# Kernel tuning notes

Measured on AMD Instinct MI355X. Metric: run time of the kernel, lower is better.

Reference implementation:

```python
import jax, jax.numpy as jnp
import numpy as np

B, S, H, A = 64, 4096, 256, 128


def entmax15(z):
    # exact entmax-1.5 along the last axis (Peters & Martins 2019)
    z = z / 2.0
    z = z - jnp.max(z, axis=-1, keepdims=True)
    zs = -jnp.sort(-z, axis=-1)                      # descending sort
    n = zs.shape[-1]
    k = jnp.arange(1, n + 1, dtype=z.dtype)
    mean = jnp.cumsum(zs, axis=-1) / k
    mean_sq = jnp.cumsum(zs * zs, axis=-1) / k
    ss = k * (mean_sq - mean * mean)
    delta = jnp.clip((1.0 - ss) / k, 0.0)
    tau = mean - jnp.sqrt(delta)
    k_star = jnp.sum(tau <= zs, axis=-1)             # support size per row
    tau_star = jnp.take_along_axis(tau, (k_star - 1)[..., None], axis=-1)
    return jnp.square(jnp.clip(z - tau_star, 0.0))


def setup_inputs() -> dict:
    key = jax.random.key(0)
    k0, k1, k2, k3, k4 = jax.random.split(key, 5)
    lim1 = 1.0 / np.sqrt(H)
    lim2 = 1.0 / np.sqrt(A)
    return {
        "lstm_output": jax.random.normal(k0, (B, S, H), dtype=jnp.float32),
        "W1": jax.random.uniform(k1, (H, A), jnp.float32, -lim1, lim1),
        "b1": jax.random.uniform(k2, (A,), jnp.float32, -lim1, lim1),
        "W2": jax.random.uniform(k3, (A, 1), jnp.float32, -lim2, lim2),
        "b2": jax.random.uniform(k4, (1,), jnp.float32, -lim2, lim2),
    }


def reference(lstm_output, W1, b1, W2, b2):
    # score MLP: Linear -> Tanh -> Linear -> squeeze(-1)  => [B, S]
    h = jnp.tanh(jnp.einsum("bsh,ha->bsa", lstm_output, W1) + b1)
    scores = (jnp.einsum("bsa,ao->bso", h, W2) + b2)[..., 0]
    weights = entmax15(scores)                       # entmax over seq axis (dim=1)
    context = jnp.einsum("bsh,bs->bh", lstm_output, weights)
    return (context, weights)
```

## Files before the change

kernel.cpp:

```cpp
#include <hip/hip_runtime.h>
#include <hip/hip_bf16.h>

#define BB 64
#define SS 4096
#define HH 256
#define AA 128
#define MT 128
#define BK 64
#define XST 72

typedef __fp16 fp16v2 __attribute__((ext_vector_type(2)));
typedef _Float16 half4v __attribute__((ext_vector_type(4)));
typedef _Float16 half8v __attribute__((ext_vector_type(8)));
typedef float floatx16 __attribute__((ext_vector_type(16)));

__device__ __forceinline__ float fast_tanh(float x) {
    float xc = fminf(fmaxf(x, -9.0f), 9.0f);
    float e = __expf(2.0f * xc);
    return 1.0f - __fdividef(2.0f, e + 1.0f);
}

__global__ void convert_w1(const float* __restrict__ W1, _Float16* __restrict__ Wt) {
    int n = blockIdx.x;
    int k = threadIdx.x;
    Wt[n * HH + k] = (_Float16)W1[k * AA + n];
}

__global__ __launch_bounds__(256) void score_mfma(
    const float* __restrict__ X,
    const _Float16* __restrict__ Wt,
    const float* __restrict__ b1,
    const float* __restrict__ W2,
    const float* __restrict__ b2,
    float* __restrict__ scores)
{
    __shared__ float smem_f[9216];
    _Float16* Xs = (_Float16*)smem_f;
    _Float16* Ws = (_Float16*)smem_f + MT * XST;
    float* part = smem_f;

    const int tid   = threadIdx.x;
    const int m0    = blockIdx.x * MT;
    const int wid   = tid >> 6;
    const int lane  = tid & 63;
    const int lrow  = lane & 31;
    const int lhalf = lane >> 5;
    const int wr    = (wid & 1) * 64;
    const int wc    = (wid >> 1) * 64;

    floatx16 acc[2][2];
    #pragma unroll
    for (int i = 0; i < 2; ++i)
        #pragma unroll
        for (int j = 0; j < 2; ++j)
            #pragma unroll
            for (int r = 0; r < 16; ++r) acc[i][j][r] = 0.0f;

    float4 xv[8];
    uint4  wvv[4];

#define LOAD_CHUNK(K0)                                                         \
    do {                                                                       \
        _Pragma("unroll")                                                      \
        for (int p = 0; p < 8; ++p) {                                          \
            int idx = tid + p * 256;                                           \
            int row = idx >> 4, c4 = idx & 15;                                 \
            xv[p] = *(const float4*)(X + (size_t)(m0 + row) * HH + (K0) + c4 * 4); \
        }                                                                      \
        _Pragma("unroll")                                                      \
        for (int p = 0; p < 4; ++p) {                                          \
            int idx = tid + p * 256;                                           \
            int n = idx >> 3, u = idx & 7;                                     \
            wvv[p] = *(const uint4*)(Wt + (size_t)n * HH + (K0) + u * 8);      \
        }                                                                      \
    } while (0)

#define STORE_CHUNK()                                                          \
    do {                                                                       \
        _Pragma("unroll")                                                      \
        for (int p = 0; p < 8; ++p) {                                          \
            int idx = tid + p * 256;                                           \
            int row = idx >> 4, c4 = idx & 15;                                 \
            union { fp16v2 h2[2]; half4v h4; } u;                              \
            u.h2[0] = __builtin_amdgcn_cvt_pkrtz(xv[p].x, xv[p].y);            \
            u.h2[1] = __builtin_amdgcn_cvt_pkrtz(xv[p].z, xv[p].w);            \
            *(half4v*)(Xs + row * XST + c4 * 4) = u.h4;                        \
        }                                                                      \
        _Pragma("unroll")                                                      \
        for (int p = 0; p < 4; ++p) {                                          \
            int idx = tid + p * 256;                                           \
            int n = idx >> 3, u2 = idx & 7;                                    \
            *(uint4*)(Ws + n * XST + u2 * 8) = wvv[p];                         \
        }                                                                      \
    } while (0)

    LOAD_CHUNK(0);
    STORE_CHUNK();
    __syncthreads();

    #pragma unroll
    for (int c = 0; c < HH / BK; ++c) {
        if (c + 1 < HH / BK) LOAD_CHUNK((c + 1) * BK);
        #pragma unroll
        for (int kk = 0; kk < BK; kk += 16) {
            half8v a0 = *(half8v*)(Xs + (wr + lrow) * XST + kk + lhalf * 8);
            half8v a1 = *(half8v*)(Xs + (wr + 32 + lrow) * XST + kk + lhalf * 8);
            half8v b0 = *(half8v*)(Ws + (wc + lrow) * XST + kk + lhalf * 8);
            half8v bq = *(half8v*)(Ws + (wc + 32 + lrow) * XST + kk + lhalf * 8);
            acc[0][0] = __builtin_amdgcn_mfma_f32_32x32x16_f16(a0, b0, acc[0][0], 0, 0, 0);
            acc[0][1] = __builtin_amdgcn_mfma_f32_32x32x16_f16(a0, bq, acc[0][1], 0, 0, 0);
            acc[1][0] = __builtin_amdgcn_mfma_f32_32x32x16_f16(a1, b0, acc[1][0], 0, 0, 0);
            acc[1][1] = __builtin_amdgcn_mfma_f32_32x32x16_f16(a1, bq, acc[1][1], 0, 0, 0);
        }
        __syncthreads();
        if (c + 1 < HH / BK) {
            STORE_CHUNK();
            __syncthreads();
        }
    }
#undef LOAD_CHUNK
#undef STORE_CHUNK

    const int cA = wc + lrow;
    const int cB = wc + 32 + lrow;
    const float b1A = b1[cA], b1B = b1[cB];
    const float w2A = W2[cA], w2B = W2[cB];
    #pragma unroll
    for (int i = 0; i < 2; ++i) {
        #pragma unroll
        for (int r = 0; r < 16; ++r) {
            float hA = fast_tanh(acc[i][0][r] + b1A) * w2A;
            float hB = fast_tanh(acc[i][1][r] + b1B) * w2B;
            int row = wr + i * 32 + (r & 3) + 8 * (r >> 2) + 4 * lhalf;
            part[row * 65 + (wid >> 1) * 32 + lrow] = hA + hB;
        }
    }
    __syncthreads();
    if (tid < MT) {
        float s = b2[0];
        #pragma unroll
        for (int c = 0; c < 64; ++c) s += part[tid * 65 + c];
        scores[m0 + tid] = s;
    }
}

__global__ __launch_bounds__(256) void entmax_kernel(
    float* __restrict__ buf, float* __restrict__ ctx)
{
    __shared__ float sred[8];
    const int b = blockIdx.x, tid = threadIdx.x;
    const int wid = tid >> 6;
    float* p = buf + (size_t)b * SS;

    float z[16];
    #pragma unroll
    for (int j = 0; j < 16; ++j) z[j] = p[tid + j * 256] * 0.5f;

    float m = -1e30f;
    #pragma unroll
    for (int j = 0; j < 16; ++j) m = fmaxf(m, z[j]);
    #pragma unroll
    for (int o = 1; o < 64; o <<= 1) m = fmaxf(m, __shfl_xor(m, o));
    if ((tid & 63) == 0) sred[wid] = m;
    __syncthreads();
    m = fmaxf(fmaxf(sred[0], sred[1]), fmaxf(sred[2], sred[3]));
    __syncthreads();
    #pragma unroll
    for (int j = 0; j < 16; ++j) z[j] -= m;

    float lo = -1.0f, hi = 0.0f;
    #pragma unroll 1
    for (int it = 0; it < 10; ++it) {
        float tau = 0.5f * (lo + hi);
        float s0 = 0.f, s1 = 0.f, s2 = 0.f, s3 = 0.f;
        #pragma unroll
        for (int j = 0; j < 16; j += 4) {
            float d0 = fmaxf(z[j]     - tau, 0.0f);
            float d1 = fmaxf(z[j + 1] - tau, 0.0f);
            float d2 = fmaxf(z[j + 2] - tau, 0.0f);
            float d3 = fmaxf(z[j + 3] - tau, 0.0f);
            s0 = fmaf(d0, d0, s0); s1 = fmaf(d1, d1, s1);
            s2 = fmaf(d2, d2, s2); s3 = fmaf(d3, d3, s3);
        }
        float s = (s0 + s1) + (s2 + s3);
        #pragma unroll
        for (int o = 1; o < 64; o <<= 1) s += __shfl_xor(s, o);
        if ((tid & 63) == 0) sred[wid] = s;
        __syncthreads();
        s = (sred[0] + sred[1]) + (sred[2] + sred[3]);
        __syncthreads();
        if (s >= 1.0f) lo = tau; else hi = tau;
    }

    float tau = lo;
    #pragma unroll 1
    for (int it = 0; it < 4; ++it) {
        float s0 = 0.f, s1 = 0.f, t0 = 0.f, t1 = 0.f;
        #pragma unroll
        for (int j = 0; j < 16; j += 2) {
            float d0 = fmaxf(z[j]     - tau, 0.0f);
            float d1 = fmaxf(z[j + 1] - tau, 0.0f);
            s0 = fmaf(d0, d0, s0); s1 = fmaf(d1, d1, s1);
            t0 += d0; t1 += d1;
        }
        float s = s0 + s1, t = t0 + t1;
        #pragma unroll
        for (int o = 1; o < 64; o <<= 1) {
            s += __shfl_xor(s, o);
            t += __shfl_xor(t, o);
        }
        if ((tid & 63) == 0) { sred[wid * 2] = s; sred[wid * 2 + 1] = t; }
        __syncthreads();
        s = (sred[0] + sred[2]) + (sred[4] + sred[6]);
        t = (sred[1] + sred[3]) + (sred[5] + sred[7]);
        __syncthreads();
        tau = fminf(tau + (s - 1.0f) / (2.0f * t + 1e-30f), hi);
    }

    #pragma unroll
    for (int j = 0; j < 16; ++j) {
        float d = fmaxf(z[j] - tau, 0.0f);
        p[tid + j * 256] = d * d;
    }
    ctx[b * HH + tid] = 0.0f;
}

__global__ __launch_bounds__(256) void context_kernel(
    const float* __restrict__ X, const float* __restrict__ w,
    float* __restrict__ ctx)
{
    const int b  = blockIdx.y;
    const int s0 = blockIdx.x * 128;
    const int h  = threadIdx.x;

    __shared__ float ws_[128];
    __shared__ int nzflag;
    if (h == 0) nzflag = 0;
    __syncthreads();
    if (h < 128) {
        float v = w[(size_t)b * SS + s0 + h];
        ws_[h] = v;
        if (v > 0.0f) nzflag = 1;
    }
    __syncthreads();
    if (!nzflag) return;

    float acc = 0.0f;
    const float* xp = X + ((size_t)b * SS + s0) * HH + h;
    #pragma unroll 4
    for (int i = 0; i < 128; ++i) {
        float wv = ws_[i];
        if (wv != 0.0f) acc = fmaf(xp[(size_t)i * HH], wv, acc);
    }
    atomicAdd(&ctx[b * HH + h], acc);
}

extern "C" void kernel_launch(void* const* d_in, const int* in_sizes, int n_in,
                              void* d_out, int out_size, void* d_ws, size_t ws_size,
                              hipStream_t stream) {
    const float* X  = (const float*)d_in[0];
    const float* W1 = (const float*)d_in[1];
    const float* b1 = (const float*)d_in[2];
    const float* W2 = (const float*)d_in[3];
    const float* b2 = (const float*)d_in[4];

    float* out = (float*)d_out;
    float* ctx = out;
    float* wts = out + BB * HH;
    _Float16* Wt = (_Float16*)d_ws;

    convert_w1<<<AA, HH, 0, stream>>>(W1, Wt);
    score_mfma<<<(BB * SS) / MT, 256, 0, stream>>>(X, Wt, b1, W2, b2, wts);
    entmax_kernel<<<BB, 256, 0, stream>>>(wts, ctx);
    context_kernel<<<dim3(SS / 128, BB), 256, 0, stream>>>(X, wts, ctx);
}
```

Before: 398.0 us.

## Fuse context reduction into entmax kernel using compacted sparse support list

Merges the entmax and context kernels into one. After computing weights, each block compacts the nonzero support indices and weights into shared memory and accumulates the context by gathering only the supported rows of X, with no global atomics and one fewer launch. It also switches the weight loads and stores to a contiguous float4 layout per thread. The cost is that the context phase now runs on only 64 blocks, so a large support would serialize the gather. It also uses 32KB of shared memory and shared-memory atomics for the compaction.

New measurement: 395.0 us. No clear change (-0.8%).

```diff
diff --git a/kernel.cpp b/kernel.cpp
--- a/kernel.cpp
+++ b/kernel.cpp
@@ -144,17 +144,28 @@
     }
 }
 
-__global__ __launch_bounds__(256) void entmax_kernel(
-    float* __restrict__ buf, float* __restrict__ ctx)
+__global__ __launch_bounds__(256) void entmax_ctx_kernel(
+    const float* __restrict__ X, float* __restrict__ buf, float* __restrict__ ctx)
 {
     __shared__ float sred[8];
+    __shared__ int   cnt;
+    __shared__ int   sidx[SS];
+    __shared__ float swt[SS];
+
     const int b = blockIdx.x, tid = threadIdx.x;
     const int wid = tid >> 6;
     float* p = buf + (size_t)b * SS;
+    const float4* p4 = (const float4*)p;
+
+    if (tid == 0) cnt = 0;
 
     float z[16];
     #pragma unroll
-    for (int j = 0; j < 16; ++j) z[j] = p[tid + j * 256] * 0.5f;
+    for (int jj = 0; jj < 4; ++jj) {
+        float4 v = p4[tid * 4 + jj];
+        z[jj * 4 + 0] = v.x * 0.5f; z[jj * 4 + 1] = v.y * 0.5f;
+        z[jj * 4 + 2] = v.z * 0.5f; z[jj * 4 + 3] = v.w * 0.5f;
+    }
 
     float m = -1e30f;
     #pragma unroll
@@ -217,42 +228,36 @@
         tau = fminf(tau + (s - 1.0f) / (2.0f * t + 1e-30f), hi);
     }
 
-    #pragma unroll
-    for (int j = 0; j < 16; ++j) {
-        float d = fmaxf(z[j] - tau, 0.0f);
-        p[tid + j * 256] = d * d;
-    }
-    ctx[b * HH + tid] = 0.0f;
-}
-
-__global__ __launch_bounds__(256) void context_kernel(
-    const float* __restrict__ X, const float* __restrict__ w,
-    float* __restrict__ ctx)
-{
-    const int b  = blockIdx.y;
-    const int s0 = blockIdx.x * 128;
-    const int h  = threadIdx.x;
-
-    __shared__ float ws_[128];
-    __shared__ int nzflag;
-    if (h == 0) nzflag = 0;
-    __syncthreads();
-    if (h < 128) {
-        float v = w[(size_t)b * SS + s0 + h];
-        ws_[h] = v;
-        if (v > 0.0f) nzflag = 1;
-    }
-    __syncthreads();
-    if (!nzflag) return;
-
-    float acc = 0.0f;
-    const float* xp = X + ((size_t)b * SS + s0) * HH + h;
-    #pragma unroll 4
-    for (int i = 0; i < 128; ++i) {
-        float wv = ws_[i];
-        if (wv != 0.0f) acc = fmaf(xp[(size_t)i * HH], wv, acc);
-    }
-    atomicAdd(&ctx[b * HH + h], acc);
+    float4* p4w = (float4*)p;
+    #pragma unroll
+    for (int jj = 0; jj < 4; ++jj) {
+        float w[4];
+        #pragma unroll
+        for (int k = 0; k < 4; ++k) {
+            float d = fmaxf(z[jj * 4 + k] - tau, 0.0f);
+            w[k] = d * d;
+            if (w[k] > 0.0f) {
+                int pos = atomicAdd(&cnt, 1);
+                sidx[pos] = tid * 16 + jj * 4 + k;
+                swt[pos]  = w[k];
+            }
+        }
+        p4w[tid * 4 + jj] = make_float4(w[0], w[1], w[2], w[3]);
+    }
+    __syncthreads();
+
+    const int n = cnt;
+    const float* xb = X + (size_t)b * SS * HH + tid;
+    float a0 = 0.f, a1 = 0.f, a2 = 0.f, a3 = 0.f;
+    int i = 0;
+    for (; i + 4 <= n; i += 4) {
+        a0 = fmaf(swt[i    ], xb[(size_t)sidx[i    ] * HH], a0);
+        a1 = fmaf(swt[i + 1], xb[(size_t)sidx[i + 1] * HH], a1);
+        a2 = fmaf(swt[i + 2], xb[(size_t)sidx[i + 2] * HH], a2);
+        a3 = fmaf(swt[i + 3], xb[(size_t)sidx[i + 3] * HH], a3);
+    }
+    for (; i < n; ++i) a0 = fmaf(swt[i], xb[(size_t)sidx[i] * HH], a0);
+    ctx[b * HH + tid] = (a0 + a1) + (a2 + a3);
 }
 
 extern "C" void kernel_launch(void* const* d_in, const int* in_sizes, int n_in,
@@ -271,6 +276,5 @@
 
     convert_w1<<<AA, HH, 0, stream>>>(W1, Wt);
     score_mfma<<<(BB * SS) / MT, 256, 0, stream>>>(X, Wt, b1, W2, b2, wts);
-    entmax_kernel<<<BB, 256, 0, stream>>>(wts, ctx);
-    context_kernel<<<dim3(SS / 128, BB), 256, 0, stream>>>(X, wts, ctx);
-}
+    entmax_ctx_kernel<<<BB, 256, 0, stream>>>(X, wts, ctx);
+}
```
